# Optimization experiments

Hardware: AMD Instinct MI355X
Metric: run time of the kernel (lower is better)

The kernel has to match this reference:

```python
import jax, jax.numpy as jnp
import numpy as np

BS, LS, NWRD, D, H, NTGT, MC = 32, 512, 100000, 128, 512, 2048, 20
TEMP = 0.5  # gumbel-softmax temperature (self.last_t)
HLOSS_COEF = 0.03


def setup_inputs() -> dict:
    key = jax.random.key(0)
    ks = jax.random.split(key, 12)
    inp_word = jax.random.randint(ks[0], (BS, LS), 0, NWRD, dtype=jnp.int32)
    inp_char = jax.random.randint(ks[1], (BS, LS, MC), 0, 95, dtype=jnp.int32)
    inp_pos = jax.random.randint(ks[2], (BS, LS), 0, 50, dtype=jnp.int32)
    keyword_table = jax.random.bernoulli(ks[3], 0.1, (NWRD,))  # wid in keywords_set
    tgt_ids = jax.random.randint(ks[4], (NTGT,), 0, NWRD, dtype=jnp.int32)
    lut = jax.random.randint(ks[5], (NWRD, MC), 0, 95, dtype=jnp.int32)
    u = jax.random.uniform(ks[6], (BS, LS, NTGT), minval=1e-6, maxval=1.0 - 1e-6)
    gumbel = -jnp.log(-jnp.log(u))  # standard Gumbel(0,1) noise
    W = jax.random.normal(ks[7], (NWRD, D), dtype=jnp.float32) * 0.02
    W1 = jax.random.normal(ks[8], (D, H), dtype=jnp.float32) * (1.0 / np.sqrt(D))
    b1 = jnp.zeros((H,), jnp.float32)
    W2 = jax.random.normal(ks[9], (H, NTGT), dtype=jnp.float32) * (1.0 / np.sqrt(H))
    b2 = jnp.zeros((NTGT,), jnp.float32)
    return dict(inp_word=inp_word, inp_char=inp_char, inp_pos=inp_pos,
                keyword_table=keyword_table, tgt_ids=tgt_ids, lut=lut,
                gumbel=gumbel, W=W, W1=W1, b1=b1, W2=W2, b2=b2)


def reference(inp_word, inp_char, inp_pos, keyword_table, tgt_ids, lut,
              gumbel, W, W1, b1, W2, b2):
    # keyword membership mask (idx in the original; torch gathers only masked
    # spots -- here we compute densely and select with the mask, same math at
    # every masked position, identity elsewhere)
    mask = keyword_table[inp_word]                      # [bs, ls] bool

    x = W[inp_word]                                     # embed: [bs, ls, d]
    hdn = jax.nn.relu(jnp.einsum('bsd,dh->bsh', x, W1) + b1)
    logits = jnp.einsum('bsh,ht->bst', hdn, W2) + b2    # [bs, ls, ntgt]

    # log_p.masked_scatter_(idx, x.max(-1)[0])
    log_p = jnp.where(mask, logits.max(axis=-1), 0.0)

    # hloss: mean entropy over masked spots * 0.03
    lsm = jax.nn.log_softmax(logits, axis=-1)
    ent = -jnp.sum(jnp.exp(lsm) * lsm, axis=-1)         # [bs, ls]
    n_spots = jnp.maximum(mask.sum(), 1)
    loss_h = (ent * mask).sum() / n_spots * HLOSS_COEF

    # gumbel_softmax(x, t): softmax((logits + g) / t)
    sft = jax.nn.softmax((logits + gumbel) / TEMP, axis=-1)  # [bs, ls, ntgt]

    # hard pick mapped through tgtwords, scattered into word
    y = tgt_ids[jnp.argmax(sft, axis=-1)]               # [bs, ls]
    word = jnp.where(mask, y, inp_word)

    # soft embedding: sft @ word_emb_tgt, word_emb_tgt = W[tgt_ids]
    x_emb = jnp.einsum('bst,td->bsd', sft, W[tgt_ids])  # [bs, ls, d]
    word_emb = jnp.where(mask[..., None], x_emb, x)     # scatter into W[word]

    char = lut[word]                                    # word_to_char lookup

    return (mask.astype(jnp.float32), log_p, word, char, word_emb, loss_h)
```

## Files before the change

kernel.cpp:

```cpp
#include <hip/hip_runtime.h>
#include <cstdint>

#define R_TOT 16384
#define T_NT  2048
#define DD    128
#define HH    512
#define MC_   20
#define BR    32
#define STEPS 64
#define NBLK  (R_TOT / BR)

#define MASK_OFF 0
#define LOGP_OFF 16384
#define WORD_OFF 32768
#define CHAR_OFF 49152
#define EMB_OFF  376832
#define LOSS_OFF 2473984

#define X_OFF     0
#define HDN_OFF   2097152
#define HDNB_OFF  10485760
#define WT_OFF    14680064
#define WTT4_OFF  14942208
#define W2T_OFF   15204352
#define W2P_OFF   16252928
#define ENT_OFF   16777216
#define CNT_OFF   16777728

typedef __attribute__((ext_vector_type(8))) short short8v;
typedef __attribute__((ext_vector_type(4))) float f32x4;
typedef unsigned short ushort_t;

__device__ __forceinline__ ushort_t f2bf(float f) {
    union { float f; unsigned int u; } v; v.f = f;
    unsigned int r = v.u + 0x7FFFu + ((v.u >> 16) & 1u);
    return (ushort_t)(r >> 16);
}

__device__ __forceinline__ void stage16(const ushort_t* gsrc, ushort_t* ldst) {
    __builtin_amdgcn_global_load_lds(
        (const __attribute__((address_space(1))) unsigned int*)gsrc,
        (__attribute__((address_space(3))) unsigned int*)ldst, 16, 0, 0);
}

__global__ __launch_bounds__(256) void k1_gather(
    const int* __restrict__ inp_word, const int* __restrict__ tgt_ids,
    const float* __restrict__ W, float* __restrict__ x, float* __restrict__ wtgt)
{
    int row = blockIdx.x * 2 + (threadIdx.x >> 7);
    int d = threadIdx.x & 127;
    if (row < R_TOT) {
        int wsrc = inp_word[row];
        x[(size_t)row * DD + d] = W[(size_t)wsrc * DD + d];
    } else {
        int rr = row - R_TOT;
        if (rr < T_NT) {
            int wsrc = tgt_ids[rr];
            wtgt[(size_t)rr * DD + d] = W[(size_t)wsrc * DD + d];
        }
    }
}

__global__ __launch_bounds__(256) void k1b_wtgtT4(
    const float* __restrict__ wtgt, ushort_t* __restrict__ wtgtT4)
{
    const int js = blockIdx.x, t = threadIdx.x;
    #pragma unroll
    for (int i = 0; i < 4; ++i) {
        int s = i * 256 + t;
        int cs = s >> 9, rem = s & 511;
        int df = rem >> 6, lane = rem & 63;
        int lrow = lane & 15, kg = lane >> 4;
        ushort_t* dst = wtgtT4 + (size_t)(((js * 2 + cs) * 8 + df) * 512 + lane * 8);
        #pragma unroll
        for (int j = 0; j < 8; ++j) {
            dst[j] = (j < 4)
                ? f2bf(wtgt[(size_t)(js * 32 + cs * 16 + kg * 4 + j) * DD + df * 16 + lrow])
                : (ushort_t)0;
        }
    }
}

__global__ __launch_bounds__(256) void k0_w2t(
    const float* __restrict__ W2, float* __restrict__ W2Tf, ushort_t* __restrict__ W2p)
{
    __shared__ float tile[32][33];
    const int js = blockIdx.x, ks = blockIdx.y;
    const int cb = js * 32, kb = ks * 32;
    const int lx = threadIdx.x & 31, ly = threadIdx.x >> 5;
    #pragma unroll
    for (int i = 0; i < 32; i += 8)
        tile[ly + i][lx] = W2[(size_t)(kb + ly + i) * T_NT + cb + lx];
    __syncthreads();
    #pragma unroll
    for (int i = 0; i < 32; i += 8) {
        int c = cb + ly + i, k = kb + lx;
        W2Tf[(size_t)c * HH + k] = tile[lx][ly + i];
    }
    if (threadIdx.x < 128) {
        int c = threadIdx.x >> 2, kgrp = threadIdx.x & 3;
        ushort_t* dst = W2p + (size_t)((js * 16 + ks) * 1024 + (c * 4 + kgrp) * 8);
        #pragma unroll
        for (int i = 0; i < 8; ++i)
            dst[i] = f2bf(tile[kgrp * 8 + i][c]);
    }
}

__global__ __launch_bounds__(256) void k2_hdn(
    const float* __restrict__ x, const float* __restrict__ W1,
    const float* __restrict__ b1, float* __restrict__ hdn, ushort_t* __restrict__ hdnB)
{
    __shared__ float As[16][64];
    __shared__ float Bs[16][64];
    const int t = threadIdx.x;
    const int bm = blockIdx.x * 64;
    const int bn = blockIdx.y * 64;
    const int tx = t & 15, ty = t >> 4;
    float acc[4][4] = {};
    for (int k0 = 0; k0 < DD; k0 += 16) {
        {
            int m = t >> 2, kq = t & 3;
            float4 v = *(const float4*)(x + (size_t)(bm + m) * DD + k0 + kq * 4);
            As[kq * 4 + 0][m] = v.x; As[kq * 4 + 1][m] = v.y;
            As[kq * 4 + 2][m] = v.z; As[kq * 4 + 3][m] = v.w;
        }
        {
            int k = t >> 4, nq = t & 15;
            *(float4*)(&Bs[k][nq * 4]) =
                *(const float4*)(W1 + (size_t)(k0 + k) * HH + bn + nq * 4);
        }
        __syncthreads();
        #pragma unroll
        for (int k = 0; k < 16; ++k) {
            float a[4], b[4];
            #pragma unroll
            for (int i = 0; i < 4; i++) a[i] = As[k][ty * 4 + i];
            #pragma unroll
            for (int j = 0; j < 4; j++) b[j] = Bs[k][tx * 4 + j];
            #pragma unroll
            for (int i = 0; i < 4; i++)
                #pragma unroll
                for (int j = 0; j < 4; j++)
                    acc[i][j] = fmaf(a[i], b[j], acc[i][j]);
        }
        __syncthreads();
    }
    #pragma unroll
    for (int i = 0; i < 4; i++) {
        int m = bm + ty * 4 + i;
        int n = bn + tx * 4;
        float4 v;
        v.x = fmaxf(acc[i][0] + b1[n + 0], 0.f);
        v.y = fmaxf(acc[i][1] + b1[n + 1], 0.f);
        v.z = fmaxf(acc[i][2] + b1[n + 2], 0.f);
        v.w = fmaxf(acc[i][3] + b1[n + 3], 0.f);
        *(float4*)(hdn + (size_t)m * HH + n) = v;
        ushort4 hb;
        hb.x = f2bf(v.x); hb.y = f2bf(v.y); hb.z = f2bf(v.z); hb.w = f2bf(v.w);
        *(ushort4*)(hdnB + (size_t)m * HH + n) = hb;
    }
}

__global__ __launch_bounds__(256) void k3_fused(
    const ushort_t* __restrict__ hdnB, const float* __restrict__ hdn,
    const ushort_t* __restrict__ W2p, const float* __restrict__ W2Tf,
    const float* __restrict__ b2, const float* __restrict__ gumbel,
    const int* __restrict__ inp_word, const int* __restrict__ keyword_table,
    const int* __restrict__ tgt_ids, const int* __restrict__ lut,
    const float* __restrict__ x, const ushort_t* __restrict__ wtgtT4,
    float* __restrict__ out, float* __restrict__ entP, float* __restrict__ cntP)
{
    __shared__ ushort_t wS[2 * 16384];
    __shared__ float pS[4][16 * 20];
    __shared__ float statC1[2 * 16 * 8];
    __shared__ int   candS[BR * 2];
    __shared__ float invs2S[BR], entS[BR];
    __shared__ int   mskS[BR];

    const int t = threadIdx.x;
    const int wid = t >> 6, lane = t & 63;
    const int Mgrp = wid >> 1, Cgrp = wid & 1;
    const int lrow = lane & 15, kgrp = lane >> 4;
    const int row0 = blockIdx.x * BR;
    const int rowA = row0 + Mgrp * 16 + lrow;

    short8v av[16];
    #pragma unroll
    for (int ks = 0; ks < 16; ++ks)
        av[ks] = *(const short8v*)(hdnB + (size_t)rowA * HH + ks * 32 + kgrp * 8);

    const ushort_t* wb = wS + ((Cgrp * 16 + lrow) * 4 + kgrp) * 8;

    const float* gp0 = gumbel + (size_t)(row0 + Mgrp * 16 + kgrp * 4 + 0) * T_NT + Cgrp * 16 + lrow;
    const float* gp1 = gp0 + T_NT;
    const float* gp2 = gp1 + T_NT;
    const float* gp3 = gp2 + T_NT;
    const float* b2p = b2 + Cgrp * 16 + lrow;
    const ushort_t* vtp = wtgtT4 + (size_t)Cgrp * 4096 + lane * 8;

    float* pw = &pS[wid][0];

    float m_[4], sE_[4], sEl_[4], s2_[4], a1_[4], a2_[4];
    int i1_[4], i2_[4];
    #pragma unroll
    for (int q = 0; q < 4; ++q) {
        m_[q] = -1e30f; sE_[q] = 0.f; sEl_[q] = 0.f; s2_[q] = 0.f;
        a1_[q] = -1e30f; a2_[q] = -1e30f; i1_[q] = 0; i2_[q] = 0;
    }
    f32x4 accpv[8];
    #pragma unroll
    for (int df = 0; df < 8; ++df) accpv[df] = (f32x4){0.f, 0.f, 0.f, 0.f};

    {
        const ushort_t* src = W2p + t * 8;
        ushort_t* dst = wS + t * 8;
        #pragma unroll
        for (int i = 0; i < 8; ++i) stage16(src + i * 2048, dst + i * 2048);
    }
    __syncthreads();

    int colv = Cgrp * 16 + lrow;

    for (int s = 0; s < STEPS; ++s) {
        const int buf = s & 1;

        if (s + 1 < STEPS) {
            const ushort_t* src = W2p + (size_t)(s + 1) * 16384 + t * 8;
            ushort_t* dst = wS + (buf ^ 1) * 16384 + t * 8;
            #pragma unroll
            for (int i = 0; i < 8; ++i) stage16(src + i * 2048, dst + i * 2048);
        }

        float g0 = *gp0, g1 = *gp1, g2 = *gp2, g3 = *gp3;
        gp0 += 32; gp1 += 32; gp2 += 32; gp3 += 32;
        float b2v = *b2p; b2p += 32;
        short8v bvf[8];
        #pragma unroll
        for (int df = 0; df < 8; ++df)
            bvf[df] = *(const short8v*)(vtp + df * 512);
        vtp += 8192;

        const ushort_t* wbb = wb + buf * 16384;
        f32x4 ac0 = (f32x4){0.f,0.f,0.f,0.f}, ac1 = ac0, ac2 = ac0, ac3 = ac0;
        #pragma unroll
        for (int ks = 0; ks < 16; ks += 4) {
            ac0 = __builtin_amdgcn_mfma_f32_16x16x32_bf16(av[ks+0], *(const short8v*)(wbb + (ks+0)*1024), ac0, 0, 0, 0);
            ac1 = __builtin_amdgcn_mfma_f32_16x16x32_bf16(av[ks+1], *(const short8v*)(wbb + (ks+1)*1024), ac1, 0, 0, 0);
            ac2 = __builtin_amdgcn_mfma_f32_16x16x32_bf16(av[ks+2], *(const short8v*)(wbb + (ks+2)*1024), ac2, 0, 0, 0);
            ac3 = __builtin_amdgcn_mfma_f32_16x16x32_bf16(av[ks+3], *(const short8v*)(wbb + (ks+3)*1024), ac3, 0, 0, 0);
        }
        f32x4 acc = (ac0 + ac1) + (ac2 + ac3);

        float g4[4] = {g0, g1, g2, g3};
        #pragma unroll
        for (int q = 0; q < 4; ++q) {
            float l = acc[q] + b2v;
            m_[q] = fmaxf(m_[q], l);
            float e1 = __expf(l);
            sE_[q] += e1; sEl_[q] = fmaf(e1, l, sEl_[q]);
            float a = l + g4[q];
            float p = __expf(2.0f * a);
            s2_[q] += p;
            if (a > a1_[q]) { a2_[q] = a1_[q]; i2_[q] = i1_[q]; a1_[q] = a; i1_[q] = colv; }
            else if (a > a2_[q]) { a2_[q] = a; i2_[q] = colv; }
            pw[(kgrp * 4 + q) * 20 + lrow] = p;
        }

        {
            float4 p4 = *(const float4*)(pw + lrow * 20 + kgrp * 4);
            short8v pav;
            pav[0] = (short)f2bf(p4.x); pav[1] = (short)f2bf(p4.y);
            pav[2] = (short)f2bf(p4.z); pav[3] = (short)f2bf(p4.w);
            pav[4] = 0; pav[5] = 0; pav[6] = 0; pav[7] = 0;
            #pragma unroll
            for (int df = 0; df < 8; ++df)
                accpv[df] = __builtin_amdgcn_mfma_f32_16x16x32_bf16(pav, bvf[df], accpv[df], 0, 0, 0);
        }

        __syncthreads();
        colv += 32;
    }

    #pragma unroll
    for (int q = 0; q < 4; ++q) {
        #pragma unroll
        for (int mk = 1; mk < 16; mk <<= 1) {
            m_[q] = fmaxf(m_[q], __shfl_xor(m_[q], mk));
            sE_[q] += __shfl_xor(sE_[q], mk);
            sEl_[q] += __shfl_xor(sEl_[q], mk);
            s2_[q] += __shfl_xor(s2_[q], mk);
            float ob1 = __shfl_xor(a1_[q], mk); int oj1 = __shfl_xor(i1_[q], mk);
            float ob2 = __shfl_xor(a2_[q], mk); int oj2 = __shfl_xor(i2_[q], mk);
            if (ob1 > a1_[q] || (ob1 == a1_[q] && oj1 < i1_[q])) {
                if (a1_[q] > ob2 || (a1_[q] == ob2 && i1_[q] < oj2)) { a2_[q] = a1_[q]; i2_[q] = i1_[q]; }
                else { a2_[q] = ob2; i2_[q] = oj2; }
                a1_[q] = ob1; i1_[q] = oj1;
            } else {
                if (ob1 > a2_[q]) { a2_[q] = ob1; i2_[q] = oj1; }
            }
        }
    }

    if (Cgrp == 1 && lrow == 0) {
        #pragma unroll
        for (int q = 0; q < 4; ++q) {
            float* st = &statC1[(Mgrp * 16 + kgrp * 4 + q) * 8];
            st[0] = m_[q]; st[1] = sE_[q]; st[2] = sEl_[q]; st[3] = s2_[q];
            st[4] = a1_[q]; st[5] = __int_as_float(i1_[q]);
            st[6] = a2_[q]; st[7] = __int_as_float(i2_[q]);
        }
    }
    float* scr = (float*)wS;
    if (Cgrp == 1) {
        #pragma unroll
        for (int df = 0; df < 8; ++df)
            #pragma unroll
            for (int q = 0; q < 4; ++q)
                scr[Mgrp * 2048 + (kgrp * 4 + q) * 128 + df * 16 + lrow] = accpv[df][q];
    }
    __syncthreads();

    if (Cgrp == 0) {
        #pragma unroll
        for (int q = 0; q < 4; ++q) {
            int r = kgrp * 4 + q;
            const float* st = &statC1[(Mgrp * 16 + r) * 8];
            float bm = st[0], bsE = st[1], bsEl = st[2], bs2 = st[3];
            float ob1 = st[4]; int oj1 = __float_as_int(st[5]);
            float ob2 = st[6]; int oj2 = __float_as_int(st[7]);
            float m = fmaxf(m_[q], bm);
            float sE = sE_[q] + bsE, sEl = sEl_[q] + bsEl, s2 = s2_[q] + bs2;
            float a1 = a1_[q], a2 = a2_[q]; int i1 = i1_[q], i2 = i2_[q];
            if (ob1 > a1 || (ob1 == a1 && oj1 < i1)) {
                if (a1 > ob2 || (a1 == ob2 && i1 < oj2)) { a2 = a1; i2 = i1; }
                else { a2 = ob2; i2 = oj2; }
                a1 = ob1; i1 = oj1;
            } else {
                if (ob1 > a2) { a2 = ob1; i2 = oj1; }
            }
            if (lrow == 0) {
                int rl = Mgrp * 16 + r;
                int grow = row0 + rl;
                int w_in = inp_word[grow];
                int msk = keyword_table[w_in] != 0;
                out[MASK_OFF + grow] = msk ? 1.0f : 0.0f;
                out[LOGP_OFF + grow] = msk ? m : 0.0f;
                invs2S[rl] = 1.0f / s2;
                mskS[rl] = msk;
                entS[rl] = msk ? (__logf(sE) - sEl / sE) : 0.0f;
                candS[rl * 2 + 0] = i1;
                candS[rl * 2 + 1] = i2;
            }
        }
        #pragma unroll
        for (int df = 0; df < 8; ++df)
            #pragma unroll
            for (int q = 0; q < 4; ++q)
                accpv[df][q] += scr[Mgrp * 2048 + (kgrp * 4 + q) * 128 + df * 16 + lrow];
    }
    __syncthreads();

    if (Cgrp == 0) {
        #pragma unroll
        for (int df = 0; df < 8; ++df) {
            #pragma unroll
            for (int q = 0; q < 4; ++q) {
                int rl = Mgrp * 16 + kgrp * 4 + q;
                int grow = row0 + rl;
                int d = df * 16 + lrow;
                float val = accpv[df][q] * invs2S[rl];
                if (!mskS[rl]) val = x[(size_t)grow * DD + d];
                out[EMB_OFF + (size_t)grow * DD + d] = val;
            }
        }
    }

    for (int rr = wid; rr < BR; rr += 4) {
        int grow = row0 + rr;
        int i1 = candS[rr * 2 + 0], i2 = candS[rr * 2 + 1];
        const float* hrow = hdn + (size_t)grow * HH;
        float4 h0 = *(const float4*)(hrow + lane * 8);
        float4 h1 = *(const float4*)(hrow + lane * 8 + 4);
        float v1, v2;
        {
            const float* wrow = W2Tf + (size_t)i1 * HH;
            float4 w0 = *(const float4*)(wrow + lane * 8);
            float4 w1 = *(const float4*)(wrow + lane * 8 + 4);
            float sdot = h0.x*w0.x + h0.y*w0.y + h0.z*w0.z + h0.w*w0.w
                       + h1.x*w1.x + h1.y*w1.y + h1.z*w1.z + h1.w*w1.w;
            #pragma unroll
            for (int mk = 1; mk < 64; mk <<= 1) sdot += __shfl_xor(sdot, mk);
            v1 = sdot + b2[i1] + gumbel[(size_t)grow * T_NT + i1];
        }
        {
            const float* wrow = W2Tf + (size_t)i2 * HH;
            float4 w0 = *(const float4*)(wrow + lane * 8);
            float4 w1 = *(const float4*)(wrow + lane * 8 + 4);
            float sdot = h0.x*w0.x + h0.y*w0.y + h0.z*w0.z + h0.w*w0.w
                       + h1.x*w1.x + h1.y*w1.y + h1.z*w1.z + h1.w*w1.w;
            #pragma unroll
            for (int mk = 1; mk < 64; mk <<= 1) sdot += __shfl_xor(sdot, mk);
            v2 = sdot + b2[i2] + gumbel[(size_t)grow * T_NT + i2];
        }
        int ibest = (v2 > v1 || (v2 == v1 && i2 < i1)) ? i2 : i1;
        int w_in = inp_word[grow];
        int msk = mskS[rr];
        int word = msk ? tgt_ids[ibest] : w_in;
        if (lane == 0) out[WORD_OFF + grow] = (float)word;
        if (lane < MC_)
            out[CHAR_OFF + (size_t)grow * MC_ + lane] = (float)lut[(size_t)word * MC_ + lane];
    }

    if (t == 0) {
        float es = 0.f; int cs = 0;
        #pragma unroll
        for (int r = 0; r < BR; r++) { es += entS[r]; cs += mskS[r]; }
        entP[blockIdx.x] = es;
        cntP[blockIdx.x] = (float)cs;
    }
}

__global__ __launch_bounds__(256) void k4_loss(
    const float* __restrict__ entP, const float* __restrict__ cntP, float* __restrict__ out)
{
    __shared__ float sE[256], sC[256];
    int t = threadIdx.x;
    float e = 0.f, c = 0.f;
    for (int i = t; i < NBLK; i += 256) { e += entP[i]; c += cntP[i]; }
    sE[t] = e; sC[t] = c;
    __syncthreads();
    for (int s = 128; s > 0; s >>= 1) {
        if (t < s) { sE[t] += sE[t + s]; sC[t] += sC[t + s]; }
        __syncthreads();
    }
    if (t == 0) {
        float ns = fmaxf(sC[0], 1.0f);
        out[LOSS_OFF] = 0.03f * sE[0] / ns;
    }
}

extern "C" void kernel_launch(void* const* d_in, const int* in_sizes, int n_in,
                              void* d_out, int out_size, void* d_ws, size_t ws_size,
                              hipStream_t stream) {
    const int* inp_word = (const int*)d_in[0];
    const int* keyword_table = (const int*)d_in[3];
    const int* tgt_ids = (const int*)d_in[4];
    const int* lut = (const int*)d_in[5];
    const float* gumbel = (const float*)d_in[6];
    const float* W = (const float*)d_in[7];
    const float* W1 = (const float*)d_in[8];
    const float* b1 = (const float*)d_in[9];
    const float* W2 = (const float*)d_in[10];
    const float* b2 = (const float*)d_in[11];
    float* out = (float*)d_out;

    float* wsf = (float*)d_ws;
    float* x = wsf + X_OFF;
    float* hdn = wsf + HDN_OFF;
    ushort_t* hdnB = (ushort_t*)(wsf + HDNB_OFF);
    float* wtgt = wsf + WT_OFF;
    ushort_t* wtgtT4 = (ushort_t*)(wsf + WTT4_OFF);
    float* W2Tf = wsf + W2T_OFF;
    ushort_t* W2p = (ushort_t*)(wsf + W2P_OFF);
    float* entP = wsf + ENT_OFF;
    float* cntP = wsf + CNT_OFF;

    k1_gather<<<(R_TOT + T_NT) / 2, 256, 0, stream>>>(inp_word, tgt_ids, W, x, wtgt);
    k1b_wtgtT4<<<64, 256, 0, stream>>>(wtgt, wtgtT4);
    k0_w2t<<<dim3(T_NT / 32, HH / 32), 256, 0, stream>>>(W2, W2Tf, W2p);
    k2_hdn<<<dim3(R_TOT / 64, HH / 64), 256, 0, stream>>>(x, W1, b1, hdn, hdnB);
    k3_fused<<<NBLK, 256, 0, stream>>>(hdnB, hdn, W2p, W2Tf, b2, gumbel,
                                       inp_word, keyword_table, tgt_ids, lut,
                                       x, wtgtT4, out, entP, cntP);
    k4_loss<<<1, 256, 0, stream>>>(entP, cntP, out);
}
```

Before: 215.8 us.

## Restructure fused logits kernel into single-wave blocks with staggered column pipeline

The main fused kernel moves from 256-thread blocks covering 32 rows to 64-thread single-wave blocks covering 16 rows, giving 1024 blocks. Each block walks all 2048 target columns itself, so the cross-wave merge of softmax and top-2 statistics through shared memory and the __syncthreads barriers go away. W2 is repacked into 16-column chunks that are double-buffered in halves, with hand-placed waitcnt fences. The starting chunk is staggered per block to spread L2 traffic. The trade-off is that every wave now streams the whole W2 alone rather than sharing each staged tile with other waves, and correctness depends on the hand-written vmcnt counts. The entropy partials are moved to reuse the wtgt scratch region.

```diff
diff --git a/kernel.cpp b/kernel.cpp
--- a/kernel.cpp
+++ b/kernel.cpp
@@ -6,9 +6,8 @@
 #define DD    128
 #define HH    512
 #define MC_   20
-#define BR    32
-#define STEPS 64
-#define NBLK  (R_TOT / BR)
+#define NSC   128
+#define NBLK  1024
 
 #define MASK_OFF 0
 #define LOGP_OFF 16384
@@ -24,8 +23,6 @@
 #define WTT4_OFF  14942208
 #define W2T_OFF   15204352
 #define W2P_OFF   16252928
-#define ENT_OFF   16777216
-#define CNT_OFF   16777728
 
 typedef __attribute__((ext_vector_type(8))) short short8v;
 typedef __attribute__((ext_vector_type(4))) float f32x4;
@@ -42,6 +39,7 @@
         (const __attribute__((address_space(1))) unsigned int*)gsrc,
         (__attribute__((address_space(3))) unsigned int*)ldst, 16, 0, 0);
 }
+#define VM_FENCE() asm volatile("" ::: "memory")
 
 __global__ __launch_bounds__(256) void k1_gather(
     const int* __restrict__ inp_word, const int* __restrict__ tgt_ids,
@@ -82,7 +80,7 @@
 }
 
 __global__ __launch_bounds__(256) void k0_w2t(
-    const float* __restrict__ W2, float* __restrict__ W2Tf, ushort_t* __restrict__ W2p)
+    const float* __restrict__ W2, float* __restrict__ W2Tf, ushort_t* __restrict__ W2p3)
 {
     __shared__ float tile[32][33];
     const int js = blockIdx.x, ks = blockIdx.y;
@@ -93,16 +91,16 @@
         tile[ly + i][lx] = W2[(size_t)(kb + ly + i) * T_NT + cb + lx];
     __syncthreads();
     #pragma unroll
-    for (int i = 0; i < 32; i += 8) {
-        int c = cb + ly + i, k = kb + lx;
-        W2Tf[(size_t)c * HH + k] = tile[lx][ly + i];
-    }
+    for (int i = 0; i < 32; i += 8)
+        W2Tf[(size_t)(cb + ly + i) * HH + kb + lx] = tile[lx][ly + i];
     if (threadIdx.x < 128) {
         int c = threadIdx.x >> 2, kgrp = threadIdx.x & 3;
-        ushort_t* dst = W2p + (size_t)((js * 16 + ks) * 1024 + (c * 4 + kgrp) * 8);
+        int cs = c >> 4, cl = c & 15;
+        ushort_t* dst = W2p3 + (size_t)(((js * 2 + cs) * 2 + (ks >> 3)) * 4096
+                                        + (ks & 7) * 512 + (cl * 4 + kgrp) * 8);
         #pragma unroll
         for (int i = 0; i < 8; ++i)
-            dst[i] = f2bf(tile[kgrp * 8 + i][c]);
+            dst[i] = f2bf(tile[kgrp * 8 + i][cb + c - cb]);
     }
 }
 
@@ -161,44 +159,38 @@
     }
 }
 
-__global__ __launch_bounds__(256) void k3_fused(
+__global__ __launch_bounds__(64, 2) void k3_fused(
     const ushort_t* __restrict__ hdnB, const float* __restrict__ hdn,
-    const ushort_t* __restrict__ W2p, const float* __restrict__ W2Tf,
+    const ushort_t* __restrict__ W2p3, const float* __restrict__ W2Tf,
     const float* __restrict__ b2, const float* __restrict__ gumbel,
     const int* __restrict__ inp_word, const int* __restrict__ keyword_table,
     const int* __restrict__ tgt_ids, const int* __restrict__ lut,
     const float* __restrict__ x, const ushort_t* __restrict__ wtgtT4,
     float* __restrict__ out, float* __restrict__ entP, float* __restrict__ cntP)
 {
-    __shared__ ushort_t wS[2 * 16384];
-    __shared__ float pS[4][16 * 20];
-    __shared__ float statC1[2 * 16 * 8];
-    __shared__ int   candS[BR * 2];
-    __shared__ float invs2S[BR], entS[BR];
-    __shared__ int   mskS[BR];
-
-    const int t = threadIdx.x;
-    const int wid = t >> 6, lane = t & 63;
-    const int Mgrp = wid >> 1, Cgrp = wid & 1;
+    __shared__ ushort_t bS[2][4096];
+    __shared__ float pS[16 * 20];
+
+    const int lane = threadIdx.x;
     const int lrow = lane & 15, kgrp = lane >> 4;
-    const int row0 = blockIdx.x * BR;
-    const int rowA = row0 + Mgrp * 16 + lrow;
+    const int row0 = blockIdx.x * 16;
 
     short8v av[16];
     #pragma unroll
     for (int ks = 0; ks < 16; ++ks)
-        av[ks] = *(const short8v*)(hdnB + (size_t)rowA * HH + ks * 32 + kgrp * 8);
-
-    const ushort_t* wb = wS + ((Cgrp * 16 + lrow) * 4 + kgrp) * 8;
-
-    const float* gp0 = gumbel + (size_t)(row0 + Mgrp * 16 + kgrp * 4 + 0) * T_NT + Cgrp * 16 + lrow;
-    const float* gp1 = gp0 + T_NT;
-    const float* gp2 = gp1 + T_NT;
-    const float* gp3 = gp2 + T_NT;
-    const float* b2p = b2 + Cgrp * 16 + lrow;
-    const ushort_t* vtp = wtgtT4 + (size_t)Cgrp * 4096 + lane * 8;
-
-    float* pw = &pS[wid][0];
+        av[ks] = *(const short8v*)(hdnB + (size_t)(row0 + lrow) * HH + ks * 32 + kgrp * 8);
+    asm volatile("s_waitcnt vmcnt(0)" ::: "memory");
+
+    const int sc0 = blockIdx.x & 127;
+
+    const ushort_t* wsrc = W2p3 + lane * 8;
+    ushort_t* dst0 = &bS[0][0] + lane * 8;
+    ushort_t* dst1 = &bS[1][0] + lane * 8;
+    const ushort_t* brd = &bS[0][0] + (lrow * 4 + kgrp) * 8;
+
+    const float* gbase = gumbel + (size_t)(row0 + kgrp * 4) * T_NT + lrow;
+    const float* b2base = b2 + lrow;
+    const ushort_t* vbase = wtgtT4 + lane * 8;
 
     float m_[4], sE_[4], sEl_[4], s2_[4], a1_[4], a2_[4];
     int i1_[4], i2_[4];
@@ -212,42 +204,65 @@
     for (int df = 0; df < 8; ++df) accpv[df] = (f32x4){0.f, 0.f, 0.f, 0.f};
 
     {
-        const ushort_t* src = W2p + t * 8;
-        ushort_t* dst = wS + t * 8;
-        #pragma unroll
-        for (int i = 0; i < 8; ++i) stage16(src + i * 2048, dst + i * 2048);
-    }
-    __syncthreads();
-
-    int colv = Cgrp * 16 + lrow;
-
-    for (int s = 0; s < STEPS; ++s) {
-        const int buf = s & 1;
-
-        if (s + 1 < STEPS) {
-            const ushort_t* src = W2p + (size_t)(s + 1) * 16384 + t * 8;
-            ushort_t* dst = wS + (buf ^ 1) * 16384 + t * 8;
-            #pragma unroll
-            for (int i = 0; i < 8; ++i) stage16(src + i * 2048, dst + i * 2048);
-        }
-
-        float g0 = *gp0, g1 = *gp1, g2 = *gp2, g3 = *gp3;
-        gp0 += 32; gp1 += 32; gp2 += 32; gp3 += 32;
-        float b2v = *b2p; b2p += 32;
+        const ushort_t* s0 = wsrc + (size_t)sc0 * 8192;
+        #pragma unroll
+        for (int i = 0; i < 8; ++i) stage16(s0 + i * 512, dst0 + i * 512);
+    }
+    VM_FENCE();
+    float g0 = gbase[(size_t)0 * T_NT + sc0 * 16];
+    float g1 = gbase[(size_t)1 * T_NT + sc0 * 16];
+    float g2 = gbase[(size_t)2 * T_NT + sc0 * 16];
+    float g3 = gbase[(size_t)3 * T_NT + sc0 * 16];
+    VM_FENCE();
+    {
+        const ushort_t* s1 = wsrc + (size_t)sc0 * 8192 + 4096;
+        #pragma unroll
+        for (int i = 0; i < 8; ++i) stage16(s1 + i * 512, dst1 + i * 512);
+    }
+    VM_FENCE();
+
+    for (int s = 0; s < NSC; ++s) {
+        const int sc = (sc0 + s) & 127;
+        const int scn = (sc0 + s + 1) & 127;
+        const int colv = sc * 16 + lrow;
+
         short8v bvf[8];
-        #pragma unroll
-        for (int df = 0; df < 8; ++df)
-            bvf[df] = *(const short8v*)(vtp + df * 512);
-        vtp += 8192;
-
-        const ushort_t* wbb = wb + buf * 16384;
+        const ushort_t* vp = vbase + (size_t)sc * 4096;
+        #pragma unroll
+        for (int df = 0; df < 8; ++df) bvf[df] = *(const short8v*)(vp + df * 512);
+        float b2v = b2base[sc * 16];
+
+        asm volatile("s_waitcnt vmcnt(21)" ::: "memory");
+
         f32x4 ac0 = (f32x4){0.f,0.f,0.f,0.f}, ac1 = ac0, ac2 = ac0, ac3 = ac0;
         #pragma unroll
-        for (int ks = 0; ks < 16; ks += 4) {
-            ac0 = __builtin_amdgcn_mfma_f32_16x16x32_bf16(av[ks+0], *(const short8v*)(wbb + (ks+0)*1024), ac0, 0, 0, 0);
-            ac1 = __builtin_amdgcn_mfma_f32_16x16x32_bf16(av[ks+1], *(const short8v*)(wbb + (ks+1)*1024), ac1, 0, 0, 0);
-            ac2 = __builtin_amdgcn_mfma_f32_16x16x32_bf16(av[ks+2], *(const short8v*)(wbb + (ks+2)*1024), ac2, 0, 0, 0);
-            ac3 = __builtin_amdgcn_mfma_f32_16x16x32_bf16(av[ks+3], *(const short8v*)(wbb + (ks+3)*1024), ac3, 0, 0, 0);
+        for (int ks = 0; ks < 8; ks += 4) {
+            ac0 = __builtin_amdgcn_mfma_f32_16x16x32_bf16(av[ks+0], *(const short8v*)(brd + (ks+0)*512), ac0, 0, 0, 0);
+            ac1 = __builtin_amdgcn_mfma_f32_16x16x32_bf16(av[ks+1], *(const short8v*)(brd + (ks+1)*512), ac1, 0, 0, 0);
+            ac2 = __builtin_amdgcn_mfma_f32_16x16x32_bf16(av[ks+2], *(const short8v*)(brd + (ks+2)*512), ac2, 0, 0, 0);
+            ac3 = __builtin_amdgcn_mfma_f32_16x16x32_bf16(av[ks+3], *(const short8v*)(brd + (ks+3)*512), ac3, 0, 0, 0);
+        }
+        asm volatile("s_waitcnt lgkmcnt(0)" ::: "memory");
+
+        {
+            const ushort_t* sn0 = wsrc + (size_t)scn * 8192;
+            #pragma unroll
+            for (int i = 0; i < 8; ++i) stage16(sn0 + i * 512, dst0 + i * 512);
+        }
+        VM_FENCE();
+        float gn0 = gbase[(size_t)0 * T_NT + scn * 16];
+        float gn1 = gbase[(size_t)1 * T_NT + scn * 16];
+        float gn2 = gbase[(size_t)2 * T_NT + scn * 16];
+        float gn3 = gbase[(size_t)3 * T_NT + scn * 16];
+
+        asm volatile("s_waitcnt vmcnt(12)" ::: "memory");
+
+        #pragma unroll
+        for (int ks = 8; ks < 16; ks += 4) {
+            ac0 = __builtin_amdgcn_mfma_f32_16x16x32_bf16(av[ks+0], *(const short8v*)(brd + 4096 + (ks-8+0)*512), ac0, 0, 0, 0);
+            ac1 = __builtin_amdgcn_mfma_f32_16x16x32_bf16(av[ks+1], *(const short8v*)(brd + 4096 + (ks-8+1)*512), ac1, 0, 0, 0);
+            ac2 = __builtin_amdgcn_mfma_f32_16x16x32_bf16(av[ks+2], *(const short8v*)(brd + 4096 + (ks-8+2)*512), ac2, 0, 0, 0);
+            ac3 = __builtin_amdgcn_mfma_f32_16x16x32_bf16(av[ks+3], *(const short8v*)(brd + 4096 + (ks-8+3)*512), ac3, 0, 0, 0);
         }
         f32x4 acc = (ac0 + ac1) + (ac2 + ac3);
 
@@ -263,11 +278,11 @@
             s2_[q] += p;
             if (a > a1_[q]) { a2_[q] = a1_[q]; i2_[q] = i1_[q]; a1_[q] = a; i1_[q] = colv; }
             else if (a > a2_[q]) { a2_[q] = a; i2_[q] = colv; }
-            pw[(kgrp * 4 + q) * 20 + lrow] = p;
-        }
-
-        {
-            float4 p4 = *(const float4*)(pw + lrow * 20 + kgrp * 4);
+            pS[(kgrp * 4 + q) * 20 + lrow] = p;
+        }
+
+        {
+            float4 p4 = *(const float4*)(&pS[lrow * 20 + kgrp * 4]);
             short8v pav;
             pav[0] = (short)f2bf(p4.x); pav[1] = (short)f2bf(p4.y);
             pav[2] = (short)f2bf(p4.z); pav[3] = (short)f2bf(p4.w);
@@ -277,8 +292,15 @@
                 accpv[df] = __builtin_amdgcn_mfma_f32_16x16x32_bf16(pav, bvf[df], accpv[df], 0, 0, 0);
         }
 
-        __syncthreads();
-        colv += 32;
+        asm volatile("s_waitcnt lgkmcnt(0)" ::: "memory");
+        {
+            const ushort_t* sn1 = wsrc + (size_t)scn * 8192 + 4096;
+            #pragma unroll
+            for (int i = 0; i < 8; ++i) stage16(sn1 + i * 512, dst1 + i * 512);
+        }
+        VM_FENCE();
+
+        g0 = gn0; g1 = gn1; g2 = gn2; g3 = gn3;
     }
 
     #pragma unroll
@@ -301,83 +323,53 @@
         }
     }
 
-    if (Cgrp == 1 && lrow == 0) {
+    float invs2_[4]; int msk_[4];
+    #pragma unroll
+    for (int q = 0; q < 4; ++q) {
+        invs2_[q] = 1.0f / s2_[q];
+        int w_in = inp_word[row0 + kgrp * 4 + q];
+        msk_[q] = keyword_table[w_in] != 0;
+    }
+
+    #pragma unroll
+    for (int df = 0; df < 8; ++df) {
         #pragma unroll
         for (int q = 0; q < 4; ++q) {
-            float* st = &statC1[(Mgrp * 16 + kgrp * 4 + q) * 8];
-            st[0] = m_[q]; st[1] = sE_[q]; st[2] = sEl_[q]; st[3] = s2_[q];
-            st[4] = a1_[q]; st[5] = __int_as_float(i1_[q]);
-            st[6] = a2_[q]; st[7] = __int_as_float(i2_[q]);
-        }
-    }
-    float* scr = (float*)wS;
-    if (Cgrp == 1) {
-        #pragma unroll
-        for (int df = 0; df < 8; ++df)
-            #pragma unroll
-            for (int q = 0; q < 4; ++q)
-                scr[Mgrp * 2048 + (kgrp * 4 + q) * 128 + df * 16 + lrow] = accpv[df][q];
-    }
-    __syncthreads();
-
-    if (Cgrp == 0) {
-        #pragma unroll
-        for (int q = 0; q < 4; ++q) {
-            int r = kgrp * 4 + q;
-            const float* st = &statC1[(Mgrp * 16 + r) * 8];
-            float bm = st[0], bsE = st[1], bsEl = st[2], bs2 = st[3];
-            float ob1 = st[4]; int oj1 = __float_as_int(st[5]);
-            float ob2 = st[6]; int oj2 = __float_as_int(st[7]);
-            float m = fmaxf(m_[q], bm);
-            float sE = sE_[q] + bsE, sEl = sEl_[q] + bsEl, s2 = s2_[q] + bs2;
-            float a1 = a1_[q], a2 = a2_[q]; int i1 = i1_[q], i2 = i2_[q];
-            if (ob1 > a1 || (ob1 == a1 && oj1 < i1)) {
-                if (a1 > ob2 || (a1 == ob2 && i1 < oj2)) { a2 = a1; i2 = i1; }
-                else { a2 = ob2; i2 = oj2; }
-                a1 = ob1; i1 = oj1;
-            } else {
-                if (ob1 > a2) { a2 = ob1; i2 = oj1; }
-            }
-            if (lrow == 0) {
-                int rl = Mgrp * 16 + r;
-                int grow = row0 + rl;
-                int w_in = inp_word[grow];
-                int msk = keyword_table[w_in] != 0;
-                out[MASK_OFF + grow] = msk ? 1.0f : 0.0f;
-                out[LOGP_OFF + grow] = msk ? m : 0.0f;
-                invs2S[rl] = 1.0f / s2;
-                mskS[rl] = msk;
-                entS[rl] = msk ? (__logf(sE) - sEl / sE) : 0.0f;
-                candS[rl * 2 + 0] = i1;
-                candS[rl * 2 + 1] = i2;
-            }
-        }
-        #pragma unroll
-        for (int df = 0; df < 8; ++df)
-            #pragma unroll
-            for (int q = 0; q < 4; ++q)
-                accpv[df][q] += scr[Mgrp * 2048 + (kgrp * 4 + q) * 128 + df * 16 + lrow];
-    }
-    __syncthreads();
-
-    if (Cgrp == 0) {
-        #pragma unroll
-        for (int df = 0; df < 8; ++df) {
-            #pragma unroll
-            for (int q = 0; q < 4; ++q) {
-                int rl = Mgrp * 16 + kgrp * 4 + q;
-                int grow = row0 + rl;
-                int d = df * 16 + lrow;
-                float val = accpv[df][q] * invs2S[rl];
-                if (!mskS[rl]) val = x[(size_t)grow * DD + d];
-                out[EMB_OFF + (size_t)grow * DD + d] = val;
-            }
-        }
-    }
-
-    for (int rr = wid; rr < BR; rr += 4) {
+            int grow = row0 + kgrp * 4 + q;
+            int d = df * 16 + lrow;
+            float val = accpv[df][q] * invs2_[q];
+            if (!msk_[q]) val = x[(size_t)grow * DD + d];
+            out[EMB_OFF + (size_t)grow * DD + d] = val;
+        }
+    }
+
+    float es = 0.f; int cs = 0;
+    #pragma unroll
+    for (int q = 0; q < 4; ++q) {
+        float entq = msk_[q] ? (__logf(sE_[q]) - sEl_[q] / sE_[q]) : 0.0f;
+        es += entq; cs += msk_[q];
+        if (lrow == 0) {
+            int grow = row0 + kgrp * 4 + q;
+            out[MASK_OFF + grow] = msk_[q] ? 1.0f : 0.0f;
+            out[LOGP_OFF + grow] = msk_[q] ? m_[q] : 0.0f;
+        }
+    }
+    {
+        float e0 = __shfl(es, 0), e16 = __shfl(es, 16), e32 = __shfl(es, 32), e48 = __shfl(es, 48);
+        int c0 = __shfl(cs, 0), c16 = __shfl(cs, 16), c32 = __shfl(cs, 32), c48 = __shfl(cs, 48);
+        if (lane == 0) {
+            entP[blockIdx.x] = e0 + e16 + e32 + e48;
+            cntP[blockIdx.x] = (float)(c0 + c16 + c32 + c48);
+        }
+    }
+
+    #pragma unroll
+    for (int rr = 0; rr < 16; ++rr) {
+        const int q = rr & 3, sl = (rr >> 2) << 4;
+        int i1 = __shfl(i1_[q], sl);
+        int i2 = __shfl(i2_[q], sl);
+        int mskr = __shfl(msk_[q], sl);
         int grow = row0 + rr;
-        int i1 = candS[rr * 2 + 0], i2 = candS[rr * 2 + 1];
         const float* hrow = hdn + (size_t)grow * HH;
         float4 h0 = *(const float4*)(hrow + lane * 8);
         float4 h1 = *(const float4*)(hrow + lane * 8 + 4);
@@ -403,20 +395,10 @@
             v2 = sdot + b2[i2] + gumbel[(size_t)grow * T_NT + i2];
         }
         int ibest = (v2 > v1 || (v2 == v1 && i2 < i1)) ? i2 : i1;
-        int w_in = inp_word[grow];
-        int msk = mskS[rr];
-        int word = msk ? tgt_ids[ibest] : w_in;
+        int word = mskr ? tgt_ids[ibest] : inp_word[grow];
         if (lane == 0) out[WORD_OFF + grow] = (float)word;
         if (lane < MC_)
             out[CHAR_OFF + (size_t)grow * MC_ + lane] = (float)lut[(size_t)word * MC_ + lane];
-    }
-
-    if (t == 0) {
-        float es = 0.f; int cs = 0;
-        #pragma unroll
-        for (int r = 0; r < BR; r++) { es += entS[r]; cs += mskS[r]; }
-        entP[blockIdx.x] = es;
-        cntP[blockIdx.x] = (float)cs;
     }
 }
 
@@ -461,16 +443,16 @@
     float* wtgt = wsf + WT_OFF;
     ushort_t* wtgtT4 = (ushort_t*)(wsf + WTT4_OFF);
     float* W2Tf = wsf + W2T_OFF;
-    ushort_t* W2p = (ushort_t*)(wsf + W2P_OFF);
-    float* entP = wsf + ENT_OFF;
-    float* cntP = wsf + CNT_OFF;
+    ushort_t* W2p3 = (ushort_t*)(wsf + W2P_OFF);
+    float* entP = wsf + WT_OFF;
+    float* cntP = wsf + WT_OFF + 1024;
 
     k1_gather<<<(R_TOT + T_NT) / 2, 256, 0, stream>>>(inp_word, tgt_ids, W, x, wtgt);
     k1b_wtgtT4<<<64, 256, 0, stream>>>(wtgt, wtgtT4);
-    k0_w2t<<<dim3(T_NT / 32, HH / 32), 256, 0, stream>>>(W2, W2Tf, W2p);
+    k0_w2t<<<dim3(T_NT / 32, HH / 32), 256, 0, stream>>>(W2, W2Tf, W2p3);
     k2_hdn<<<dim3(R_TOT / 64, HH / 64), 256, 0, stream>>>(x, W1, b1, hdn, hdnB);
-    k3_fused<<<NBLK, 256, 0, stream>>>(hdnB, hdn, W2p, W2Tf, b2, gumbel,
-                                       inp_word, keyword_table, tgt_ids, lut,
-                                       x, wtgtT4, out, entP, cntP);
+    k3_fused<<<NBLK, 64, 0, stream>>>(hdnB, hdn, W2p3, W2Tf, b2, gumbel,
+                                      inp_word, keyword_table, tgt_ids, lut,
+                                      x, wtgtT4, out, entP, cntP);
     k4_loss<<<1, 256, 0, stream>>>(entP, cntP, out);
 }
```

After: 294.7 us. +36.6%, slower.

## Split target columns across waves with 16-row blocks and direct-from-global W2 loads

Applied to the files above, without the earlier changes.

The fused logits/softmax kernel now processes 16 rows per block (1024 blocks). Each of the four waves sweeps a rotated subset of 32 column chunks, and the per-wave softmax, top-2 and P·V partials are merged at the end through shared memory. The double-buffered LDS staging of W2 with per-step block barriers is replaced by per-wave direct global loads of a retiled W2p, and A operands are staged once into LDS. This aims to raise occupancy (launch bounds 4 blocks) and remove per-step synchronisation. In exchange it relies on cache for W2 reuse and adds a four-way merge.

```diff
diff --git a/kernel.cpp b/kernel.cpp
--- a/kernel.cpp
+++ b/kernel.cpp
@@ -6,9 +6,9 @@
 #define DD    128
 #define HH    512
 #define MC_   20
-#define BR    32
-#define STEPS 64
-#define NBLK  (R_TOT / BR)
+#define NBLK  1024
+#define NSC   128
+#define SPW   32
 
 #define MASK_OFF 0
 #define LOGP_OFF 16384
@@ -24,8 +24,6 @@
 #define WTT4_OFF  14942208
 #define W2T_OFF   15204352
 #define W2P_OFF   16252928
-#define ENT_OFF   16777216
-#define CNT_OFF   16777728
 
 typedef __attribute__((ext_vector_type(8))) short short8v;
 typedef __attribute__((ext_vector_type(4))) float f32x4;
@@ -35,12 +33,6 @@
     union { float f; unsigned int u; } v; v.f = f;
     unsigned int r = v.u + 0x7FFFu + ((v.u >> 16) & 1u);
     return (ushort_t)(r >> 16);
-}
-
-__device__ __forceinline__ void stage16(const ushort_t* gsrc, ushort_t* ldst) {
-    __builtin_amdgcn_global_load_lds(
-        (const __attribute__((address_space(1))) unsigned int*)gsrc,
-        (__attribute__((address_space(3))) unsigned int*)ldst, 16, 0, 0);
 }
 
 __global__ __launch_bounds__(256) void k1_gather(
@@ -85,24 +77,23 @@
     const float* __restrict__ W2, float* __restrict__ W2Tf, ushort_t* __restrict__ W2p)
 {
     __shared__ float tile[32][33];
-    const int js = blockIdx.x, ks = blockIdx.y;
-    const int cb = js * 32, kb = ks * 32;
+    const int jc = blockIdx.x, jk = blockIdx.y;
+    const int cb = jc * 32, kb = jk * 32;
     const int lx = threadIdx.x & 31, ly = threadIdx.x >> 5;
     #pragma unroll
     for (int i = 0; i < 32; i += 8)
         tile[ly + i][lx] = W2[(size_t)(kb + ly + i) * T_NT + cb + lx];
     __syncthreads();
     #pragma unroll
-    for (int i = 0; i < 32; i += 8) {
-        int c = cb + ly + i, k = kb + lx;
-        W2Tf[(size_t)c * HH + k] = tile[lx][ly + i];
-    }
+    for (int i = 0; i < 32; i += 8)
+        W2Tf[(size_t)(cb + ly + i) * HH + kb + lx] = tile[lx][ly + i];
     if (threadIdx.x < 128) {
-        int c = threadIdx.x >> 2, kgrp = threadIdx.x & 3;
-        ushort_t* dst = W2p + (size_t)((js * 16 + ks) * 1024 + (c * 4 + kgrp) * 8);
-        #pragma unroll
-        for (int i = 0; i < 8; ++i)
-            dst[i] = f2bf(tile[kgrp * 8 + i][c]);
+        int cs = threadIdx.x >> 6, lane = threadIdx.x & 63;
+        int lrow = lane & 15, kgrp = lane >> 4;
+        ushort_t* dst = W2p + (size_t)((cb / 16 + cs) * 16 + jk) * 512 + lane * 8;
+        #pragma unroll
+        for (int j = 0; j < 8; ++j)
+            dst[j] = f2bf(tile[kgrp * 8 + j][cs * 16 + lrow]);
     }
 }
 
@@ -161,7 +152,7 @@
     }
 }
 
-__global__ __launch_bounds__(256) void k3_fused(
+__global__ __launch_bounds__(256, 4) void k3_fused(
     const ushort_t* __restrict__ hdnB, const float* __restrict__ hdn,
     const ushort_t* __restrict__ W2p, const float* __restrict__ W2Tf,
     const float* __restrict__ b2, const float* __restrict__ gumbel,
@@ -170,34 +161,37 @@
     const float* __restrict__ x, const ushort_t* __restrict__ wtgtT4,
     float* __restrict__ out, float* __restrict__ entP, float* __restrict__ cntP)
 {
-    __shared__ ushort_t wS[2 * 16384];
+    __shared__ float bigS[6144];
     __shared__ float pS[4][16 * 20];
-    __shared__ float statC1[2 * 16 * 8];
-    __shared__ int   candS[BR * 2];
-    __shared__ float invs2S[BR], entS[BR];
-    __shared__ int   mskS[BR];
+    __shared__ float statP[4][16][8];
+    __shared__ int   candS[16 * 2];
+    __shared__ int   mskS[16];
 
     const int t = threadIdx.x;
     const int wid = t >> 6, lane = t & 63;
-    const int Mgrp = wid >> 1, Cgrp = wid & 1;
     const int lrow = lane & 15, kgrp = lane >> 4;
-    const int row0 = blockIdx.x * BR;
-    const int rowA = row0 + Mgrp * 16 + lrow;
-
-    short8v av[16];
-    #pragma unroll
-    for (int ks = 0; ks < 16; ++ks)
-        av[ks] = *(const short8v*)(hdnB + (size_t)rowA * HH + ks * 32 + kgrp * 8);
-
-    const ushort_t* wb = wS + ((Cgrp * 16 + lrow) * 4 + kgrp) * 8;
-
-    const float* gp0 = gumbel + (size_t)(row0 + Mgrp * 16 + kgrp * 4 + 0) * T_NT + Cgrp * 16 + lrow;
-    const float* gp1 = gp0 + T_NT;
-    const float* gp2 = gp1 + T_NT;
-    const float* gp3 = gp2 + T_NT;
-    const float* b2p = b2 + Cgrp * 16 + lrow;
-    const ushort_t* vtp = wtgtT4 + (size_t)Cgrp * 4096 + lane * 8;
-
+    const int row0 = blockIdx.x * 16;
+
+    ushort_t* aP = (ushort_t*)bigS;
+
+    #pragma unroll
+    for (int i = 0; i < 4; ++i) {
+        int gid = i * 256 + t;
+        int ks = gid >> 6, l2 = gid & 63;
+        int lr = l2 & 15, kg = l2 >> 4;
+        uint4 v = *(const uint4*)(hdnB + (size_t)(row0 + lr) * HH + ks * 32 + kg * 8);
+        *(uint4*)(aP + gid * 8) = v;
+    }
+    __syncthreads();
+
+    const ushort_t* aLane = aP + lane * 8;
+
+    const int base_sc = ((blockIdx.x & 31) * 4 + wid) & 127;
+    const float* gq[4];
+    #pragma unroll
+    for (int q = 0; q < 4; ++q)
+        gq[q] = gumbel + (size_t)(row0 + kgrp * 4 + q) * T_NT + lrow;
+    const float* b2p = b2 + lrow;
     float* pw = &pS[wid][0];
 
     float m_[4], sE_[4], sEl_[4], s2_[4], a1_[4], a2_[4];
@@ -211,47 +205,36 @@
     #pragma unroll
     for (int df = 0; df < 8; ++df) accpv[df] = (f32x4){0.f, 0.f, 0.f, 0.f};
 
-    {
-        const ushort_t* src = W2p + t * 8;
-        ushort_t* dst = wS + t * 8;
-        #pragma unroll
-        for (int i = 0; i < 8; ++i) stage16(src + i * 2048, dst + i * 2048);
-    }
-    __syncthreads();
-
-    int colv = Cgrp * 16 + lrow;
-
-    for (int s = 0; s < STEPS; ++s) {
-        const int buf = s & 1;
-
-        if (s + 1 < STEPS) {
-            const ushort_t* src = W2p + (size_t)(s + 1) * 16384 + t * 8;
-            ushort_t* dst = wS + (buf ^ 1) * 16384 + t * 8;
-            #pragma unroll
-            for (int i = 0; i < 8; ++i) stage16(src + i * 2048, dst + i * 2048);
-        }
-
-        float g0 = *gp0, g1 = *gp1, g2 = *gp2, g3 = *gp3;
-        gp0 += 32; gp1 += 32; gp2 += 32; gp3 += 32;
-        float b2v = *b2p; b2p += 32;
+    float gc0 = gq[0][base_sc * 16], gc1 = gq[1][base_sc * 16];
+    float gc2 = gq[2][base_sc * 16], gc3 = gq[3][base_sc * 16];
+
+    int scc = base_sc;
+    for (int s = 0; s < SPW; ++s) {
+        const int scn = (scc + 4) & 127;
+        float b2v = b2p[scc * 16];
+
+        const ushort_t* bp = W2p + (size_t)scc * 8192 + lane * 8;
+        f32x4 c[4];
+        #pragma unroll
+        for (int j = 0; j < 4; ++j) c[j] = (f32x4){0.f, 0.f, 0.f, 0.f};
+        #pragma unroll
+        for (int ks = 0; ks < 16; ++ks) {
+            short8v a = *(const short8v*)(aLane + ks * 512);
+            short8v b = *(const short8v*)(bp + ks * 512);
+            c[ks & 3] = __builtin_amdgcn_mfma_f32_16x16x32_bf16(a, b, c[ks & 3], 0, 0, 0);
+        }
+        f32x4 acc = (c[0] + c[1]) + (c[2] + c[3]);
+
+        float gn0 = gq[0][scn * 16], gn1 = gq[1][scn * 16];
+        float gn2 = gq[2][scn * 16], gn3 = gq[3][scn * 16];
+
+        const ushort_t* vp = wtgtT4 + (size_t)scc * 4096 + lane * 8;
         short8v bvf[8];
         #pragma unroll
-        for (int df = 0; df < 8; ++df)
-            bvf[df] = *(const short8v*)(vtp + df * 512);
-        vtp += 8192;
-
-        const ushort_t* wbb = wb + buf * 16384;
-        f32x4 ac0 = (f32x4){0.f,0.f,0.f,0.f}, ac1 = ac0, ac2 = ac0, ac3 = ac0;
-        #pragma unroll
-        for (int ks = 0; ks < 16; ks += 4) {
-            ac0 = __builtin_amdgcn_mfma_f32_16x16x32_bf16(av[ks+0], *(const short8v*)(wbb + (ks+0)*1024), ac0, 0, 0, 0);
-            ac1 = __builtin_amdgcn_mfma_f32_16x16x32_bf16(av[ks+1], *(const short8v*)(wbb + (ks+1)*1024), ac1, 0, 0, 0);
-            ac2 = __builtin_amdgcn_mfma_f32_16x16x32_bf16(av[ks+2], *(const short8v*)(wbb + (ks+2)*1024), ac2, 0, 0, 0);
-            ac3 = __builtin_amdgcn_mfma_f32_16x16x32_bf16(av[ks+3], *(const short8v*)(wbb + (ks+3)*1024), ac3, 0, 0, 0);
-        }
-        f32x4 acc = (ac0 + ac1) + (ac2 + ac3);
-
-        float g4[4] = {g0, g1, g2, g3};
+        for (int df = 0; df < 8; ++df) bvf[df] = *(const short8v*)(vp + df * 512);
+
+        const int colv = scc * 16 + lrow;
+        float g4[4] = {gc0, gc1, gc2, gc3};
         #pragma unroll
         for (int q = 0; q < 4; ++q) {
             float l = acc[q] + b2v;
@@ -277,8 +260,8 @@
                 accpv[df] = __builtin_amdgcn_mfma_f32_16x16x32_bf16(pav, bvf[df], accpv[df], 0, 0, 0);
         }
 
-        __syncthreads();
-        colv += 32;
+        gc0 = gn0; gc1 = gn1; gc2 = gn2; gc3 = gn3;
+        scc = scn;
     }
 
     #pragma unroll
@@ -301,83 +284,95 @@
         }
     }
 
-    if (Cgrp == 1 && lrow == 0) {
+    __syncthreads();
+
+    if (lrow == 0) {
         #pragma unroll
         for (int q = 0; q < 4; ++q) {
-            float* st = &statC1[(Mgrp * 16 + kgrp * 4 + q) * 8];
+            float* st = &statP[wid][kgrp * 4 + q][0];
             st[0] = m_[q]; st[1] = sE_[q]; st[2] = sEl_[q]; st[3] = s2_[q];
             st[4] = a1_[q]; st[5] = __int_as_float(i1_[q]);
             st[6] = a2_[q]; st[7] = __int_as_float(i2_[q]);
         }
     }
-    float* scr = (float*)wS;
-    if (Cgrp == 1) {
+    if (wid >= 1) {
+        float* scr = bigS + (wid - 1) * 2048;
         #pragma unroll
         for (int df = 0; df < 8; ++df)
             #pragma unroll
             for (int q = 0; q < 4; ++q)
-                scr[Mgrp * 2048 + (kgrp * 4 + q) * 128 + df * 16 + lrow] = accpv[df][q];
-    }
-    __syncthreads();
-
-    if (Cgrp == 0) {
+                scr[(kgrp * 4 + q) * 128 + df * 16 + lrow] = accpv[df][q];
+    }
+    __syncthreads();
+
+    if (wid == 0) {
+        float invs2_[4]; int msk_[4];
+        float es = 0.f; int cs = 0;
         #pragma unroll
         for (int q = 0; q < 4; ++q) {
             int r = kgrp * 4 + q;
-            const float* st = &statC1[(Mgrp * 16 + r) * 8];
-            float bm = st[0], bsE = st[1], bsEl = st[2], bs2 = st[3];
-            float ob1 = st[4]; int oj1 = __float_as_int(st[5]);
-            float ob2 = st[6]; int oj2 = __float_as_int(st[7]);
-            float m = fmaxf(m_[q], bm);
-            float sE = sE_[q] + bsE, sEl = sEl_[q] + bsEl, s2 = s2_[q] + bs2;
-            float a1 = a1_[q], a2 = a2_[q]; int i1 = i1_[q], i2 = i2_[q];
-            if (ob1 > a1 || (ob1 == a1 && oj1 < i1)) {
-                if (a1 > ob2 || (a1 == ob2 && i1 < oj2)) { a2 = a1; i2 = i1; }
-                else { a2 = ob2; i2 = oj2; }
-                a1 = ob1; i1 = oj1;
-            } else {
-                if (ob1 > a2) { a2 = ob1; i2 = oj1; }
+            float M = m_[q], SE = sE_[q], SEL = sEl_[q], S2 = s2_[q];
+            float A1 = a1_[q], A2 = a2_[q]; int I1 = i1_[q], I2 = i2_[q];
+            #pragma unroll
+            for (int w = 1; w < 4; ++w) {
+                const float* st = &statP[w][r][0];
+                float ob1 = st[4]; int oj1 = __float_as_int(st[5]);
+                float ob2 = st[6]; int oj2 = __float_as_int(st[7]);
+                M = fmaxf(M, st[0]); SE += st[1]; SEL += st[2]; S2 += st[3];
+                if (ob1 > A1 || (ob1 == A1 && oj1 < I1)) {
+                    if (A1 > ob2 || (A1 == ob2 && I1 < oj2)) { A2 = A1; I2 = I1; }
+                    else { A2 = ob2; I2 = oj2; }
+                    A1 = ob1; I1 = oj1;
+                } else {
+                    if (ob1 > A2) { A2 = ob1; I2 = oj1; }
+                }
             }
+            invs2_[q] = 1.0f / S2;
+            int grow = row0 + r;
+            int w_in = inp_word[grow];
+            int msk = keyword_table[w_in] != 0;
+            msk_[q] = msk;
+            float entq = msk ? (__logf(SE) - SEL / SE) : 0.0f;
+            es += entq; cs += msk;
             if (lrow == 0) {
-                int rl = Mgrp * 16 + r;
-                int grow = row0 + rl;
-                int w_in = inp_word[grow];
-                int msk = keyword_table[w_in] != 0;
                 out[MASK_OFF + grow] = msk ? 1.0f : 0.0f;
-                out[LOGP_OFF + grow] = msk ? m : 0.0f;
-                invs2S[rl] = 1.0f / s2;
-                mskS[rl] = msk;
-                entS[rl] = msk ? (__logf(sE) - sEl / sE) : 0.0f;
-                candS[rl * 2 + 0] = i1;
-                candS[rl * 2 + 1] = i2;
+                out[LOGP_OFF + grow] = msk ? M : 0.0f;
+                mskS[r] = msk;
+                candS[r * 2 + 0] = I1;
+                candS[r * 2 + 1] = I2;
             }
         }
-        #pragma unroll
-        for (int df = 0; df < 8; ++df)
-            #pragma unroll
-            for (int q = 0; q < 4; ++q)
-                accpv[df][q] += scr[Mgrp * 2048 + (kgrp * 4 + q) * 128 + df * 16 + lrow];
-    }
-    __syncthreads();
-
-    if (Cgrp == 0) {
+        {
+            float e0 = __shfl(es, 0), e16 = __shfl(es, 16), e32 = __shfl(es, 32), e48 = __shfl(es, 48);
+            int c0 = __shfl(cs, 0), c16 = __shfl(cs, 16), c32 = __shfl(cs, 32), c48 = __shfl(cs, 48);
+            if (lane == 0) {
+                entP[blockIdx.x] = e0 + e16 + e32 + e48;
+                cntP[blockIdx.x] = (float)(c0 + c16 + c32 + c48);
+            }
+        }
         #pragma unroll
         for (int df = 0; df < 8; ++df) {
             #pragma unroll
             for (int q = 0; q < 4; ++q) {
-                int rl = Mgrp * 16 + kgrp * 4 + q;
-                int grow = row0 + rl;
+                int r = kgrp * 4 + q;
+                float v = accpv[df][q]
+                        + bigS[0 * 2048 + r * 128 + df * 16 + lrow]
+                        + bigS[1 * 2048 + r * 128 + df * 16 + lrow]
+                        + bigS[2 * 2048 + r * 128 + df * 16 + lrow];
+                int grow = row0 + r;
                 int d = df * 16 + lrow;
-                float val = accpv[df][q] * invs2S[rl];
-                if (!mskS[rl]) val = x[(size_t)grow * DD + d];
+                float val = v * invs2_[q];
+                if (!msk_[q]) val = x[(size_t)grow * DD + d];
                 out[EMB_OFF + (size_t)grow * DD + d] = val;
             }
         }
     }
-
-    for (int rr = wid; rr < BR; rr += 4) {
+    __syncthreads();
+
+    for (int rr = wid; rr < 16; rr += 4) {
         int grow = row0 + rr;
         int i1 = candS[rr * 2 + 0], i2 = candS[rr * 2 + 1];
+        int mskr = mskS[rr];
         const float* hrow = hdn + (size_t)grow * HH;
         float4 h0 = *(const float4*)(hrow + lane * 8);
         float4 h1 = *(const float4*)(hrow + lane * 8 + 4);
@@ -403,20 +398,10 @@
             v2 = sdot + b2[i2] + gumbel[(size_t)grow * T_NT + i2];
         }
         int ibest = (v2 > v1 || (v2 == v1 && i2 < i1)) ? i2 : i1;
-        int w_in = inp_word[grow];
-        int msk = mskS[rr];
-        int word = msk ? tgt_ids[ibest] : w_in;
+        int word = mskr ? tgt_ids[ibest] : inp_word[grow];
         if (lane == 0) out[WORD_OFF + grow] = (float)word;
         if (lane < MC_)
             out[CHAR_OFF + (size_t)grow * MC_ + lane] = (float)lut[(size_t)word * MC_ + lane];
-    }
-
-    if (t == 0) {
-        float es = 0.f; int cs = 0;
-        #pragma unroll
-        for (int r = 0; r < BR; r++) { es += entS[r]; cs += mskS[r]; }
-        entP[blockIdx.x] = es;
-        cntP[blockIdx.x] = (float)cs;
     }
 }
 
@@ -462,8 +447,8 @@
     ushort_t* wtgtT4 = (ushort_t*)(wsf + WTT4_OFF);
     float* W2Tf = wsf + W2T_OFF;
     ushort_t* W2p = (ushort_t*)(wsf + W2P_OFF);
-    float* entP = wsf + ENT_OFF;
-    float* cntP = wsf + CNT_OFF;
+    float* entP = wsf + WT_OFF;
+    float* cntP = wsf + WT_OFF + 1024;
 
     k1_gather<<<(R_TOT + T_NT) / 2, 256, 0, stream>>>(inp_word, tgt_ids, W, x, wtgt);
     k1b_wtgtT4<<<64, 256, 0, stream>>>(wtgt, wtgtT4);
```

New measurement: 747.7 us. +246.5%, slower.
